# Kernel optimization log

Hardware: AMD Instinct MI355X
Metric: run time of the kernel (lower is better)

The kernel has to match this reference:

```python
import jax, jax.numpy as jnp
import numpy as np

D_MODEL = 1024
NUM_HEADS = 16
HEAD_DIM = D_MODEL // NUM_HEADS


def setup_inputs() -> dict:
    key = jax.random.key(0)
    ks = jax.random.split(key, 5)
    B, T = 4, 2048
    x = jax.random.normal(ks[0], (B, T, D_MODEL), dtype=jnp.float32)
    s = 1.0 / np.sqrt(D_MODEL)
    w_qkv = jax.random.normal(ks[1], (D_MODEL, 3 * D_MODEL), dtype=jnp.float32) * s
    b_qkv = jnp.zeros((3 * D_MODEL,), dtype=jnp.float32)
    w_out = jax.random.normal(ks[2], (D_MODEL, D_MODEL), dtype=jnp.float32) * s
    b_out = jnp.zeros((D_MODEL,), dtype=jnp.float32)
    return {"x": x, "w_qkv": w_qkv, "b_qkv": b_qkv, "w_out": w_out, "b_out": b_out}


def reference(x, w_qkv, b_qkv, w_out, b_out):
    B, T, C = x.shape
    H, Dh = NUM_HEADS, HEAD_DIM
    qkv = x @ w_qkv + b_qkv                      # [B,T,3C]
    qkv = qkv.reshape(B, T, 3, H, Dh)
    q = qkv[:, :, 0].transpose(0, 2, 1, 3)      # [B,H,T,Dh]
    k = qkv[:, :, 1].transpose(0, 2, 1, 3)
    v = qkv[:, :, 2].transpose(0, 2, 1, 3)
    scale = 1.0 / np.sqrt(Dh)
    attn = jnp.einsum('bhqd,bhkd->bhqk', q, k) * scale  # [B,H,T,T]
    causal = jnp.tril(jnp.ones((T, T), dtype=bool))
    attn = jnp.where(causal[None, None], attn, -jnp.inf)
    attn = jax.nn.softmax(attn, axis=-1)
    out = jnp.einsum('bhqk,bhkd->bhqd', attn, v)        # [B,H,T,Dh]
    out = out.transpose(0, 2, 1, 3).reshape(B, T, C)
    return out @ w_out + b_out
```

## Files before the change

kernel.cpp:

```cpp
#include <hip/hip_runtime.h>
#include <stdint.h>

typedef unsigned short u16;
typedef __attribute__((ext_vector_type(8))) __bf16 bf16x8;
typedef __attribute__((ext_vector_type(4))) float f32x4;
typedef __attribute__((ext_vector_type(4))) u16 u16x4;
typedef __attribute__((ext_vector_type(4))) uint32_t u32x4;

__device__ __forceinline__ u16 f2bf(float f) {
    union { float f; uint32_t u; } v; v.f = f;
    uint32_t r = (v.u + 0x7fffu + ((v.u >> 16) & 1u)) >> 16;
    return (u16)r;
}

__device__ __forceinline__ void gll16(const u16* g, u16* l) {
    __builtin_amdgcn_global_load_lds((const __attribute__((address_space(1))) uint32_t*)g,
                                     (__attribute__((address_space(3))) uint32_t*)l, 16, 0, 0);
}

__global__ void cast_kernel(const float* __restrict__ in, u16* __restrict__ out, int n) {
    int i = (blockIdx.x * blockDim.x + threadIdx.x) * 4;
    if (i + 3 < n) {
        float4 v = *(const float4*)(in + i);
        u16x4 o;
        o.x = f2bf(v.x); o.y = f2bf(v.y); o.z = f2bf(v.z); o.w = f2bf(v.w);
        *(u16x4*)(out + i) = o;
    }
}

__global__ void transpose_cast(const float* __restrict__ in, u16* __restrict__ out, int R, int C) {
    __shared__ float tile[32][33];
    int c0 = blockIdx.x * 32;
    int r0 = blockIdx.y * 32;
    int tx = threadIdx.x, ty = threadIdx.y;
#pragma unroll
    for (int i = 0; i < 32; i += 8)
        tile[ty + i][tx] = in[(size_t)(r0 + ty + i) * C + c0 + tx];
    __syncthreads();
#pragma unroll
    for (int i = 0; i < 32; i += 8)
        out[(size_t)(c0 + ty + i) * R + r0 + tx] = f2bf(tile[tx][ty + i]);
}

template <int EPI>
__global__ __launch_bounds__(256) void gemm_bt(
    const u16* __restrict__ A, const u16* __restrict__ Bt,
    int K, int N, const float* __restrict__ bias,
    u16* __restrict__ Qb, u16* __restrict__ Kb, u16* __restrict__ Vtb,
    float* __restrict__ Cout)
{
    __shared__ __align__(16) u16 smem[EPI == 0 ? 18432 : 16384];

    const int tid  = threadIdx.x;
    const int lane = tid & 63;
    const int wave = tid >> 6;
    const int wm = (wave >> 1) * 64;
    const int wn = (wave & 1) * 64;
    const int l15 = lane & 15;
    const int l4  = lane >> 4;
    const int bm = blockIdx.x * 128;
    const int bn = blockIdx.y * 128;

    f32x4 acc[4][4];
#pragma unroll
    for (int i = 0; i < 4; i++)
#pragma unroll
        for (int j = 0; j < 4; j++)
            acc[i][j] = (f32x4){0.f, 0.f, 0.f, 0.f};

    const int r0 = tid >> 2;
    const int u0 = (tid & 3) ^ ((r0 >> 1) & 3);
    const u16* Ap = A + (size_t)(bm + r0) * K + u0 * 8;
    const u16* Bp = Bt + (size_t)(bn + r0) * K + u0 * 8;
    const int su = (l15 >> 1) & 3;

    auto stage = [&](int k0, int pb) {
        u16* dst = smem + pb * 8192 + wave * 512;
        gll16(Ap + k0, dst);
        gll16(Ap + (size_t)64 * K + k0, dst + 2048);
        gll16(Bp + k0, dst + 4096);
        gll16(Bp + (size_t)64 * K + k0, dst + 6144);
    };

    stage(0, 0);
    __syncthreads();

    int p = 0;
    for (int k0 = 0; k0 < K; k0 += 32) {
        if (k0 + 32 < K) stage(k0 + 32, p ^ 1);

        const u16* AsP = smem + p * 8192;
        const u16* BsP = AsP + 4096;

        bf16x8 af[4];
#pragma unroll
        for (int mi = 0; mi < 4; mi++)
            af[mi] = *(const bf16x8*)&AsP[(wm + mi * 16 + l15) * 32 + ((l4 ^ su) * 8)];
#pragma unroll
        for (int ni = 0; ni < 4; ni++) {
            bf16x8 bf = *(const bf16x8*)&BsP[(wn + ni * 16 + l15) * 32 + ((l4 ^ su) * 8)];
#pragma unroll
            for (int mi = 0; mi < 4; mi++)
                acc[mi][ni] = __builtin_amdgcn_mfma_f32_16x16x32_bf16(af[mi], bf, acc[mi][ni], 0, 0, 0);
        }

        __syncthreads();
        p ^= 1;
    }

    if (EPI == 0 && blockIdx.y >= 16) {
        u16* tr = smem + wave * (64 * 72);
#pragma unroll
        for (int mi = 0; mi < 4; mi++)
#pragma unroll
            for (int ni = 0; ni < 4; ni++)
#pragma unroll
                for (int r = 0; r < 4; r++) {
                    int d  = ni * 16 + l15;
                    int tl = mi * 16 + l4 * 4 + r;
                    int gn = bn + wn + ni * 16 + l15;
                    tr[d * 72 + tl] = f2bf(acc[mi][ni][r] + bias[gn]);
                }
        __syncthreads();
        const int hh = (bn + wn - 2048) >> 6;
        const int bb = (bm + wm) >> 11;
        const int tglob0 = (bm + wm) & 2047;
        const int t0 = (lane & 7) * 8;
#pragma unroll
        for (int it = 0; it < 8; it++) {
            int d = it * 8 + (lane >> 3);
            uint4 v = *(const uint4*)&tr[d * 72 + t0];
            *(uint4*)(Vtb + (((size_t)(bb * 16 + hh)) * 64 + d) * 2048 + tglob0 + t0) = v;
        }
        return;
    }

#pragma unroll
    for (int mi = 0; mi < 4; mi++) {
#pragma unroll
        for (int ni = 0; ni < 4; ni++) {
#pragma unroll
            for (int r = 0; r < 4; r++) {
                int gm = bm + wm + mi * 16 + l4 * 4 + r;
                int gn = bn + wn + ni * 16 + l15;
                float v = acc[mi][ni][r] + bias[gn];
                if (EPI == 0) {
                    int s = gn >> 10, rem = gn & 1023;
                    int h = rem >> 6, d = rem & 63;
                    int b = gm >> 11, t = gm & 2047;
                    size_t qkidx = (((size_t)(b * 16 + h)) * 2048 + t) * 64 + d;
                    if (s == 0)      Qb[qkidx] = f2bf(v * 0.125f);
                    else             Kb[qkidx] = f2bf(v);
                } else {
                    Cout[(size_t)gm * N + gn] = v;
                }
            }
        }
    }
}

__global__ __launch_bounds__(256) void attn_kernel(
    const u16* __restrict__ Qb, const u16* __restrict__ Kb,
    const u16* __restrict__ Vtb, u16* __restrict__ Ob)
{
    const int blk = blockIdx.x;
    const int qb  = 15 - (blk >> 6);
    const int bh  = blk & 63;
    const int b   = bh >> 4;
    const int h   = bh & 15;
    const u16* Qh = Qb + ((size_t)bh) * 2048 * 64;
    const u16* Kh = Kb + ((size_t)bh) * 2048 * 64;
    const u16* Vh = Vtb + ((size_t)bh) * 64 * 2048;

    __shared__ __align__(16) u16 KsBuf[2][64 * 64];
    __shared__ __align__(16) u16 VsBuf[2][64 * 64];

    const int tid  = threadIdx.x;
    const int wave = tid >> 6;
    const int lane = tid & 63;
    const int l15 = lane & 15;
    const int l4  = lane >> 4;

    const int addr_a = (((l4 & 1) * 32) + l15) * 4;
    const int addr_b = addr_a + 64;
    const bool hi_t  = (l4 & 2) != 0;

    const bf16x8 ones = __builtin_bit_cast(bf16x8,
        (u32x4){0x3F803F80u, 0x3F803F80u, 0x3F803F80u, 0x3F803F80u});

    const int qrow0 = qb * 128 + wave * 32;
    const int nt = 2 * (qb + 1);

    auto stage = [&](int j, int pb) {
#pragma unroll
        for (int i = 0; i < 2; i++) {
            int lu = i * 256 + tid;
            int r = lu >> 3, u = (lu & 7) ^ (r & 7);
            gll16(Kh + ((size_t)(j * 64 + r)) * 64 + u * 8,
                  &KsBuf[pb][(i * 256 + wave * 64) * 8]);
            gll16(Vh + (size_t)r * 2048 + j * 64 + u * 8,
                  &VsBuf[pb][(i * 256 + wave * 64) * 8]);
        }
    };

    bf16x8 qf[2][2];
#pragma unroll
    for (int mi = 0; mi < 2; mi++)
#pragma unroll
        for (int kd = 0; kd < 2; kd++)
            qf[mi][kd] = *(const bf16x8*)(Qh + (size_t)(qrow0 + mi * 16 + l15) * 64 + kd * 32 + l4 * 8);

    f32x4 Ot[4][2];
#pragma unroll
    for (int md = 0; md < 4; md++)
#pragma unroll
        for (int mi = 0; mi < 2; mi++)
            Ot[md][mi] = (f32x4){0.f, 0.f, 0.f, 0.f};
    f32x4 L[2];
    L[0] = (f32x4){0.f, 0.f, 0.f, 0.f};
    L[1] = (f32x4){0.f, 0.f, 0.f, 0.f};

    stage(0, 0);
    __syncthreads();

    int p = 0;
    for (int j = 0; j < nt; ++j) {
        if (j + 1 < nt) stage(j + 1, p ^ 1);

        const u16* Kc = KsBuf[p];
        const u16* Vc = VsBuf[p];
        const int kvb = j * 64 - qb * 128;
        const bool diag = (kvb >= 0);

#pragma unroll
        for (int kk = 0; kk < 2; kk++) {
            uint32_t pk[2][2][2];
#pragma unroll
            for (int tt = 0; tt < 2; tt++) {
                const int t = kk * 2 + tt;
                const int rr = t * 16 + l15;
                f32x4 St[2];
                St[0] = (f32x4){0.f, 0.f, 0.f, 0.f};
                St[1] = (f32x4){0.f, 0.f, 0.f, 0.f};
#pragma unroll
                for (int kd = 0; kd < 2; kd++) {
                    bf16x8 kf = *(const bf16x8*)&Kc[((rr << 3) + ((kd * 4 + l4) ^ (rr & 7))) * 8];
                    St[0] = __builtin_amdgcn_mfma_f32_16x16x32_bf16(kf, qf[0][kd], St[0], 0, 0, 0);
                    St[1] = __builtin_amdgcn_mfma_f32_16x16x32_bf16(kf, qf[1][kd], St[1], 0, 0, 0);
                }
#pragma unroll
                for (int mi = 0; mi < 2; mi++) {
                    int qloc = wave * 32 + mi * 16 + l15;
                    float pr[4];
#pragma unroll
                    for (int r = 0; r < 4; r++) {
                        float s = St[mi][r];
                        if (diag) {
                            int kvloc = kvb + t * 16 + l4 * 4 + r;
                            if (kvloc > qloc) s = -__builtin_inff();
                        }
                        pr[r] = __expf(s);
                    }
                    union { float f; uint32_t u; } u0, u1, u2, u3;
                    u0.f = pr[0]; u1.f = pr[1]; u2.f = pr[2]; u3.f = pr[3];
                    pk[tt][mi][0] = __builtin_amdgcn_perm(u1.u, u0.u, 0x07060302u);
                    pk[tt][mi][1] = __builtin_amdgcn_perm(u3.u, u2.u, 0x07060302u);
                }
            }

            bf16x8 vtf[4];
#pragma unroll
            for (int md = 0; md < 4; md++) {
                const int rr = md * 16 + l15;
                vtf[md] = *(const bf16x8*)&Vc[((rr << 3) + ((kk * 4 + l4) ^ (rr & 7))) * 8];
            }
#pragma unroll
            for (int mi = 0; mi < 2; mi++) {
                uint32_t s0a = __builtin_amdgcn_ds_bpermute(addr_a, pk[0][mi][0]);
                uint32_t s0b = __builtin_amdgcn_ds_bpermute(addr_a, pk[1][mi][0]);
                uint32_t s1a = __builtin_amdgcn_ds_bpermute(addr_a, pk[0][mi][1]);
                uint32_t s1b = __builtin_amdgcn_ds_bpermute(addr_a, pk[1][mi][1]);
                uint32_t s2a = __builtin_amdgcn_ds_bpermute(addr_b, pk[0][mi][0]);
                uint32_t s2b = __builtin_amdgcn_ds_bpermute(addr_b, pk[1][mi][0]);
                uint32_t s3a = __builtin_amdgcn_ds_bpermute(addr_b, pk[0][mi][1]);
                uint32_t s3b = __builtin_amdgcn_ds_bpermute(addr_b, pk[1][mi][1]);
                u32x4 pt;
                pt.x = hi_t ? s0b : s0a;
                pt.y = hi_t ? s1b : s1a;
                pt.z = hi_t ? s2b : s2a;
                pt.w = hi_t ? s3b : s3a;
                bf16x8 ptf = __builtin_bit_cast(bf16x8, pt);
#pragma unroll
                for (int md = 0; md < 4; md++)
                    Ot[md][mi] = __builtin_amdgcn_mfma_f32_16x16x32_bf16(vtf[md], ptf, Ot[md][mi], 0, 0, 0);
                L[mi] = __builtin_amdgcn_mfma_f32_16x16x32_bf16(ones, ptf, L[mi], 0, 0, 0);
            }
        }

        __syncthreads();
        p ^= 1;
    }

#pragma unroll
    for (int mi = 0; mi < 2; mi++) {
        float inv = 1.0f / L[mi][0];
        int t = qrow0 + mi * 16 + l15;
#pragma unroll
        for (int md = 0; md < 4; md++) {
            u16x4 o;
            o.x = f2bf(Ot[md][mi][0] * inv);
            o.y = f2bf(Ot[md][mi][1] * inv);
            o.z = f2bf(Ot[md][mi][2] * inv);
            o.w = f2bf(Ot[md][mi][3] * inv);
            *(u16x4*)(Ob + ((size_t)(b * 2048 + t)) * 1024 + h * 64 + md * 16 + l4 * 4) = o;
        }
    }
}

extern "C" void kernel_launch(void* const* d_in, const int* in_sizes, int n_in,
                              void* d_out, int out_size, void* d_ws, size_t ws_size,
                              hipStream_t stream) {
    const float* x     = (const float*)d_in[0];
    const float* w_qkv = (const float*)d_in[1];
    const float* b_qkv = (const float*)d_in[2];
    const float* w_out = (const float*)d_in[3];
    const float* b_out = (const float*)d_in[4];
    float* out = (float*)d_out;

    size_t off = 0;
    char* ws = (char*)d_ws;
    auto alloc = [&](size_t bytes) -> void* {
        void* p = ws + off;
        off += (bytes + 255) & ~(size_t)255;
        return p;
    };
    u16* xb    = (u16*)alloc((size_t)8192 * 1024 * 2);
    u16* wqkvT = (u16*)alloc((size_t)3072 * 1024 * 2);
    u16* woutT = (u16*)alloc((size_t)1024 * 1024 * 2);
    u16* Qb    = (u16*)alloc((size_t)8192 * 1024 * 2);
    u16* Kb    = (u16*)alloc((size_t)8192 * 1024 * 2);
    u16* Vtb   = (u16*)alloc((size_t)8192 * 1024 * 2);
    u16* Ob    = xb;

    cast_kernel<<<dim3(8192), dim3(256), 0, stream>>>(x, xb, 8192 * 1024);
    transpose_cast<<<dim3(3072 / 32, 1024 / 32), dim3(32, 8), 0, stream>>>(w_qkv, wqkvT, 1024, 3072);
    transpose_cast<<<dim3(1024 / 32, 1024 / 32), dim3(32, 8), 0, stream>>>(w_out, woutT, 1024, 1024);

    gemm_bt<0><<<dim3(64, 24), dim3(256), 0, stream>>>(xb, wqkvT, 1024, 3072, b_qkv, Qb, Kb, Vtb, nullptr);
    attn_kernel<<<dim3(1024), dim3(256), 0, stream>>>(Qb, Kb, Vtb, Ob);
    gemm_bt<1><<<dim3(64, 8), dim3(256), 0, stream>>>(Ob, woutT, 1024, 1024, b_out, nullptr, nullptr, nullptr, out);
}
```

Before: 252.6 us.

## Rewrite attention inner loop with 32x32x16 MFMA and register-resident P

```diff
diff --git a/kernel.cpp b/kernel.cpp
--- a/kernel.cpp
+++ b/kernel.cpp
@@ -4,8 +4,10 @@
 typedef unsigned short u16;
 typedef __attribute__((ext_vector_type(8))) __bf16 bf16x8;
 typedef __attribute__((ext_vector_type(4))) float f32x4;
+typedef __attribute__((ext_vector_type(16))) float f32x16;
 typedef __attribute__((ext_vector_type(4))) u16 u16x4;
 typedef __attribute__((ext_vector_type(4))) uint32_t u32x4;
+typedef __attribute__((ext_vector_type(2))) uint32_t u32x2;
 
 __device__ __forceinline__ u16 f2bf(float f) {
     union { float f; uint32_t u; } v; v.f = f;
@@ -159,7 +161,7 @@
     }
 }
 
-__global__ __launch_bounds__(256) void attn_kernel(
+__global__ __launch_bounds__(256, 4) void attn_kernel(
     const u16* __restrict__ Qb, const u16* __restrict__ Kb,
     const u16* __restrict__ Vtb, u16* __restrict__ Ob)
 {
@@ -167,26 +169,19 @@
     const int qb  = 15 - (blk >> 6);
     const int bh  = blk & 63;
     const int b   = bh >> 4;
-    const int h   = bh & 15;
+    const int hd  = bh & 15;
     const u16* Qh = Qb + ((size_t)bh) * 2048 * 64;
     const u16* Kh = Kb + ((size_t)bh) * 2048 * 64;
     const u16* Vh = Vtb + ((size_t)bh) * 64 * 2048;
 
-    __shared__ __align__(16) u16 KsBuf[2][64 * 64];
-    __shared__ __align__(16) u16 VsBuf[2][64 * 64];
+    __shared__ __align__(16) u16 KsBuf[2][4096];
+    __shared__ __align__(16) u16 VsBuf[2][4096];
 
     const int tid  = threadIdx.x;
     const int wave = tid >> 6;
     const int lane = tid & 63;
-    const int l15 = lane & 15;
-    const int l4  = lane >> 4;
-
-    const int addr_a = (((l4 & 1) * 32) + l15) * 4;
-    const int addr_b = addr_a + 64;
-    const bool hi_t  = (l4 & 2) != 0;
-
-    const bf16x8 ones = __builtin_bit_cast(bf16x8,
-        (u32x4){0x3F803F80u, 0x3F803F80u, 0x3F803F80u, 0x3F803F80u});
+    const int l31  = lane & 31;
+    const int hl   = lane >> 5;
 
     const int qrow0 = qb * 128 + wave * 32;
     const int nt = 2 * (qb + 1);
@@ -195,30 +190,28 @@
 #pragma unroll
         for (int i = 0; i < 2; i++) {
             int lu = i * 256 + tid;
-            int r = lu >> 3, u = (lu & 7) ^ (r & 7);
-            gll16(Kh + ((size_t)(j * 64 + r)) * 64 + u * 8,
+            int mr = lu >> 4;
+            int u  = (lu & 15) ^ (mr & 15);
+            int rr = mr * 2 + (u >> 3), uc = u & 7;
+            gll16(Kh + ((size_t)(j * 64 + rr)) * 64 + uc * 8,
                   &KsBuf[pb][(i * 256 + wave * 64) * 8]);
-            gll16(Vh + (size_t)r * 2048 + j * 64 + u * 8,
+            gll16(Vh + (size_t)rr * 2048 + j * 64 + uc * 8,
                   &VsBuf[pb][(i * 256 + wave * 64) * 8]);
         }
     };
 
-    bf16x8 qf[2][2];
-#pragma unroll
-    for (int mi = 0; mi < 2; mi++)
-#pragma unroll
-        for (int kd = 0; kd < 2; kd++)
-            qf[mi][kd] = *(const bf16x8*)(Qh + (size_t)(qrow0 + mi * 16 + l15) * 64 + kd * 32 + l4 * 8);
-
-    f32x4 Ot[4][2];
-#pragma unroll
-    for (int md = 0; md < 4; md++)
-#pragma unroll
-        for (int mi = 0; mi < 2; mi++)
-            Ot[md][mi] = (f32x4){0.f, 0.f, 0.f, 0.f};
-    f32x4 L[2];
-    L[0] = (f32x4){0.f, 0.f, 0.f, 0.f};
-    L[1] = (f32x4){0.f, 0.f, 0.f, 0.f};
+    bf16x8 qf[4];
+#pragma unroll
+    for (int c = 0; c < 4; c++)
+        qf[c] = *(const bf16x8*)(Qh + (size_t)(qrow0 + l31) * 64 + c * 16 + hl * 8);
+
+    f32x16 Ot[2];
+#pragma unroll
+    for (int dblk = 0; dblk < 2; dblk++)
+#pragma unroll
+        for (int r = 0; r < 16; r++)
+            Ot[dblk][r] = 0.f;
+    float la[4] = {0.f, 0.f, 0.f, 0.f};
 
     stage(0, 0);
     __syncthreads();
@@ -231,69 +224,70 @@
         const u16* Vc = VsBuf[p];
         const int kvb = j * 64 - qb * 128;
         const bool diag = (kvb >= 0);
-
-#pragma unroll
-        for (int kk = 0; kk < 2; kk++) {
-            uint32_t pk[2][2][2];
-#pragma unroll
-            for (int tt = 0; tt < 2; tt++) {
-                const int t = kk * 2 + tt;
-                const int rr = t * 16 + l15;
-                f32x4 St[2];
-                St[0] = (f32x4){0.f, 0.f, 0.f, 0.f};
-                St[1] = (f32x4){0.f, 0.f, 0.f, 0.f};
-#pragma unroll
-                for (int kd = 0; kd < 2; kd++) {
-                    bf16x8 kf = *(const bf16x8*)&Kc[((rr << 3) + ((kd * 4 + l4) ^ (rr & 7))) * 8];
-                    St[0] = __builtin_amdgcn_mfma_f32_16x16x32_bf16(kf, qf[0][kd], St[0], 0, 0, 0);
-                    St[1] = __builtin_amdgcn_mfma_f32_16x16x32_bf16(kf, qf[1][kd], St[1], 0, 0, 0);
-                }
-#pragma unroll
-                for (int mi = 0; mi < 2; mi++) {
-                    int qloc = wave * 32 + mi * 16 + l15;
-                    float pr[4];
-#pragma unroll
-                    for (int r = 0; r < 4; r++) {
-                        float s = St[mi][r];
-                        if (diag) {
-                            int kvloc = kvb + t * 16 + l4 * 4 + r;
-                            if (kvloc > qloc) s = -__builtin_inff();
-                        }
-                        pr[r] = __expf(s);
+        const int qq = wave * 32 + l31;
+        const bool skip = diag && (kvb > wave * 32 + 31);
+
+        if (!skip) {
+#pragma unroll
+            for (int s = 0; s < 2; s++) {
+                f32x16 S;
+#pragma unroll
+                for (int r = 0; r < 16; r++) S[r] = 0.f;
+                const int kv_l = s * 32 + l31;
+                const int mrK  = kv_l >> 1;
+                const int ubK  = ((kv_l & 1) << 3) + hl;
+#pragma unroll
+                for (int c = 0; c < 4; c++) {
+                    bf16x8 kf = *(const bf16x8*)&Kc[((mrK << 4) + ((ubK + c * 2) ^ (mrK & 15))) << 3];
+                    S = __builtin_amdgcn_mfma_f32_32x32x16_bf16(kf, qf[c], S, 0, 0, 0);
+                }
+
+                u32x2 vl[2][2], vh[2][2];
+                const int dd0 = l31;
+#pragma unroll
+                for (int dblk = 0; dblk < 2; dblk++) {
+                    int dd  = dblk * 32 + dd0;
+                    int mrV = dd >> 1;
+                    int ubV = (dd & 1) << 3;
+#pragma unroll
+                    for (int f = 0; f < 2; f++) {
+                        int uc0 = 4 * s + 2 * f;
+                        vl[dblk][f] = *(const u32x2*)&Vc[(((mrV << 4) + ((ubV + uc0) ^ (mrV & 15))) << 3) + hl * 4];
+                        vh[dblk][f] = *(const u32x2*)&Vc[(((mrV << 4) + ((ubV + uc0 + 1) ^ (mrV & 15))) << 3) + hl * 4];
                     }
-                    union { float f; uint32_t u; } u0, u1, u2, u3;
-                    u0.f = pr[0]; u1.f = pr[1]; u2.f = pr[2]; u3.f = pr[3];
-                    pk[tt][mi][0] = __builtin_amdgcn_perm(u1.u, u0.u, 0x07060302u);
-                    pk[tt][mi][1] = __builtin_amdgcn_perm(u3.u, u2.u, 0x07060302u);
-                }
-            }
-
-            bf16x8 vtf[4];
-#pragma unroll
-            for (int md = 0; md < 4; md++) {
-                const int rr = md * 16 + l15;
-                vtf[md] = *(const bf16x8*)&Vc[((rr << 3) + ((kk * 4 + l4) ^ (rr & 7))) * 8];
-            }
-#pragma unroll
-            for (int mi = 0; mi < 2; mi++) {
-                uint32_t s0a = __builtin_amdgcn_ds_bpermute(addr_a, pk[0][mi][0]);
-                uint32_t s0b = __builtin_amdgcn_ds_bpermute(addr_a, pk[1][mi][0]);
-                uint32_t s1a = __builtin_amdgcn_ds_bpermute(addr_a, pk[0][mi][1]);
-                uint32_t s1b = __builtin_amdgcn_ds_bpermute(addr_a, pk[1][mi][1]);
-                uint32_t s2a = __builtin_amdgcn_ds_bpermute(addr_b, pk[0][mi][0]);
-                uint32_t s2b = __builtin_amdgcn_ds_bpermute(addr_b, pk[1][mi][0]);
-                uint32_t s3a = __builtin_amdgcn_ds_bpermute(addr_b, pk[0][mi][1]);
-                uint32_t s3b = __builtin_amdgcn_ds_bpermute(addr_b, pk[1][mi][1]);
-                u32x4 pt;
-                pt.x = hi_t ? s0b : s0a;
-                pt.y = hi_t ? s1b : s1a;
-                pt.z = hi_t ? s2b : s2a;
-                pt.w = hi_t ? s3b : s3a;
-                bf16x8 ptf = __builtin_bit_cast(bf16x8, pt);
-#pragma unroll
-                for (int md = 0; md < 4; md++)
-                    Ot[md][mi] = __builtin_amdgcn_mfma_f32_16x16x32_bf16(vtf[md], ptf, Ot[md][mi], 0, 0, 0);
-                L[mi] = __builtin_amdgcn_mfma_f32_16x16x32_bf16(ones, ptf, L[mi], 0, 0, 0);
+                }
+
+                float pr[16];
+#pragma unroll
+                for (int r = 0; r < 16; r++) {
+                    float sv = S[r];
+                    if (diag) {
+                        int kvloc = s * 32 + (r & 3) + 8 * (r >> 2) + 4 * hl;
+                        if (kvb + kvloc > qq) sv = -__builtin_inff();
+                    }
+                    pr[r] = __expf(sv);
+                    la[r & 3] += pr[r];
+                }
+
+                uint32_t w[8];
+#pragma unroll
+                for (int t = 0; t < 8; t++) {
+                    union { float fv; uint32_t u; } e0, e1;
+                    e0.fv = pr[2 * t]; e1.fv = pr[2 * t + 1];
+                    w[t] = __builtin_amdgcn_perm(e1.u, e0.u, 0x07060302u);
+                }
+
+#pragma unroll
+                for (int f = 0; f < 2; f++) {
+                    bf16x8 ptf = __builtin_bit_cast(bf16x8,
+                        (u32x4){w[4 * f + 0], w[4 * f + 1], w[4 * f + 2], w[4 * f + 3]});
+#pragma unroll
+                    for (int dblk = 0; dblk < 2; dblk++) {
+                        bf16x8 vtf = __builtin_bit_cast(bf16x8,
+                            (u32x4){vl[dblk][f].x, vl[dblk][f].y, vh[dblk][f].x, vh[dblk][f].y});
+                        Ot[dblk] = __builtin_amdgcn_mfma_f32_32x32x16_bf16(vtf, ptf, Ot[dblk], 0, 0, 0);
+                    }
+                }
             }
         }
 
@@ -301,20 +295,22 @@
         p ^= 1;
     }
 
-#pragma unroll
-    for (int mi = 0; mi < 2; mi++) {
-        float inv = 1.0f / L[mi][0];
-        int t = qrow0 + mi * 16 + l15;
-#pragma unroll
-        for (int md = 0; md < 4; md++) {
+    float Lh = (la[0] + la[1]) + (la[2] + la[3]);
+    float Lo = __shfl_xor(Lh, 32);
+    float inv = 1.0f / (Lh + Lo);
+
+    const int tq = qrow0 + l31;
+#pragma unroll
+    for (int dblk = 0; dblk < 2; dblk++)
+#pragma unroll
+        for (int g = 0; g < 4; g++) {
             u16x4 o;
-            o.x = f2bf(Ot[md][mi][0] * inv);
-            o.y = f2bf(Ot[md][mi][1] * inv);
-            o.z = f2bf(Ot[md][mi][2] * inv);
-            o.w = f2bf(Ot[md][mi][3] * inv);
-            *(u16x4*)(Ob + ((size_t)(b * 2048 + t)) * 1024 + h * 64 + md * 16 + l4 * 4) = o;
-        }
-    }
+            o.x = f2bf(Ot[dblk][g * 4 + 0] * inv);
+            o.y = f2bf(Ot[dblk][g * 4 + 1] * inv);
+            o.z = f2bf(Ot[dblk][g * 4 + 2] * inv);
+            o.w = f2bf(Ot[dblk][g * 4 + 3] * inv);
+            *(u16x4*)(Ob + ((size_t)(b * 2048 + tq)) * 1024 + hd * 64 + dblk * 32 + g * 8 + hl * 4) = o;
+        }
 }
 
 extern "C" void kernel_launch(void* const* d_in, const int* in_sizes, int n_in,
```

Measured after the change: 270.8 us. 7.2% more time.
